# Kernel optimization log

Hardware: AMD Instinct MI355X
Metric: run time of the kernel (lower is better)

## Reference

```python
import jax, jax.numpy as jnp
import numpy as np

E, D, H = 8, 512, 2048  # num_experts, features, features*mlp_ratio
B, S = 4, 512


def _lecun(key, shape):
    fan_in = shape[-2] if len(shape) >= 2 else shape[0]
    return jax.random.normal(key, shape, dtype=jnp.float32) / jnp.sqrt(jnp.float32(fan_in))


def setup_inputs() -> dict:
    key = jax.random.key(0)
    ks = jax.random.split(key, 8)
    return {
        'x_real': jax.random.normal(ks[0], (B, S, D), dtype=jnp.float32),
        'x_imag': jax.random.normal(ks[1], (B, S, D), dtype=jnp.float32),
        # gating Dense over concat([amp, phase]) -> in_features = 2*D
        'gate_W': _lecun(ks[2], (2 * D, E)),
        'gate_b': jnp.zeros((E,), jnp.float32),
        # per-expert ComplexLinear 1: D -> H
        'W1r': _lecun(ks[3], (E, D, H)),
        'W1i': _lecun(ks[4], (E, D, H)),
        'b1r': jnp.zeros((E, H), jnp.float32),
        'b1i': jnp.zeros((E, H), jnp.float32),
        # per-expert ComplexModReLU bias
        'mod_b': jnp.zeros((E, H), jnp.float32),
        # per-expert ComplexLinear 2: H -> D
        'W2r': _lecun(ks[5], (E, H, D)),
        'W2i': _lecun(ks[6], (E, H, D)),
        'b2r': jnp.zeros((E, D), jnp.float32),
        'b2i': jnp.zeros((E, D), jnp.float32),
    }


def reference(x_real, x_imag, gate_W, gate_b, W1r, W1i, b1r, b1i, mod_b, W2r, W2i, b2r, b2i):
    eps = 1e-10
    # --- gating: scores over [|z|, angle(z)] ---
    amp = jnp.sqrt(x_real ** 2 + x_imag ** 2)            # |z|, [B,S,D]
    phase = jnp.arctan2(x_imag, x_real)                  # angle(z)
    routing_input = jnp.concatenate([amp, phase], axis=-1)  # [B,S,2D]
    scores = routing_input @ gate_W + gate_b             # [B,S,E]
    probs = jax.nn.softmax(scores, axis=-1)
    idx = jnp.argmax(probs, axis=-1)                     # [B,S] top-1 expert

    # --- all experts dense (faithful to reference): complex linear 1 ---
    # (Wr + iWi)(xr + ixi) : hr = xr Wr - xi Wi ; hi = xr Wi + xi Wr
    h_r = (jnp.einsum('bsd,edh->ebsh', x_real, W1r)
           - jnp.einsum('bsd,edh->ebsh', x_imag, W1i)) + b1r[:, None, None, :]
    h_i = (jnp.einsum('bsd,edh->ebsh', x_real, W1i)
           + jnp.einsum('bsd,edh->ebsh', x_imag, W1r)) + b1i[:, None, None, :]

    # --- ComplexModReLU: relu(|z|+b) * z / (|z|+eps), |z| = sqrt(r^2+i^2+eps) ---
    a = jnp.sqrt(h_r ** 2 + h_i ** 2 + eps)              # [E,B,S,H]
    scale = jax.nn.relu(a + mod_b[:, None, None, :]) / (a + eps)
    h_r = h_r * scale
    h_i = h_i * scale

    # --- complex linear 2 ---
    o_r = (jnp.einsum('ebsh,ehd->ebsd', h_r, W2r)
           - jnp.einsum('ebsh,ehd->ebsd', h_i, W2i)) + b2r[:, None, None, :]
    o_i = (jnp.einsum('ebsh,ehd->ebsd', h_r, W2i)
           + jnp.einsum('ebsh,ehd->ebsd', h_i, W2r)) + b2i[:, None, None, :]

    # --- mask + weight (top-1): out = sum_e out_e * probs[...,e] * (argmax==e) ---
    e_ids = jnp.arange(probs.shape[-1])
    w = jnp.transpose(probs, (2, 0, 1)) * (idx[None, :, :] == e_ids[:, None, None])  # [E,B,S]
    out_r = jnp.einsum('ebs,ebsd->bsd', w, o_r)
    out_i = jnp.einsum('ebs,ebsd->bsd', w, o_i)
    return (out_r, out_i)
```

## Files before the change

kernel.cpp:

```cpp
#include <hip/hip_runtime.h>
#include <math.h>

#define NE 8
#define ND 512
#define NH 2048
#define NT 2048

typedef __attribute__((ext_vector_type(8))) short short8;
typedef __attribute__((ext_vector_type(4))) float f32x4;

#define GLL(g, d) __builtin_amdgcn_global_load_lds( \
    (const __attribute__((address_space(1))) void*)(g), \
    (__attribute__((address_space(3))) void*)(d), 16, 0, 0)

__device__ __forceinline__ unsigned short f2bf(float x) {
    unsigned int u = __builtin_bit_cast(unsigned int, x);
    u += 0x7FFFu + ((u >> 16) & 1u);
    return (unsigned short)(u >> 16);
}

__device__ __forceinline__ short8 neg8(short8 v) {
    int4 u = __builtin_bit_cast(int4, v);
    u.x ^= 0x80008000; u.y ^= 0x80008000; u.z ^= 0x80008000; u.w ^= 0x80008000;
    return __builtin_bit_cast(short8, u);
}

__device__ __forceinline__ short8 lds8(const unsigned short* p) {
    return *(const short8*)p;
}

__global__ __launch_bounds__(256) void gate_kernel(
    const float* __restrict__ xr, const float* __restrict__ xi,
    const float* __restrict__ gW, const float* __restrict__ gb,
    float* __restrict__ gate_w,
    int* __restrict__ counts, int* __restrict__ tok_list)
{
    int t = blockIdx.x;
    int tid = threadIdx.x;
    const float* xrt = xr + (size_t)t * ND;
    const float* xit = xi + (size_t)t * ND;

    float acc[NE] = {0,0,0,0,0,0,0,0};
    for (int r = tid; r < 2 * ND; r += 256) {
        int d = r & (ND - 1);
        float a = xrt[d], b = xit[d];
        float v = (r < ND) ? sqrtf(a * a + b * b) : atan2f(b, a);
        const float4* g = (const float4*)(gW + (size_t)r * NE);
        float4 g0 = g[0], g1 = g[1];
        acc[0] += v * g0.x; acc[1] += v * g0.y; acc[2] += v * g0.z; acc[3] += v * g0.w;
        acc[4] += v * g1.x; acc[5] += v * g1.y; acc[6] += v * g1.z; acc[7] += v * g1.w;
    }
    #pragma unroll
    for (int e = 0; e < NE; e++) {
        for (int off = 32; off > 0; off >>= 1)
            acc[e] += __shfl_down(acc[e], off, 64);
    }
    __shared__ float part[4][NE];
    int wave = tid >> 6, lane = tid & 63;
    if (lane == 0) {
        #pragma unroll
        for (int e = 0; e < NE; e++) part[wave][e] = acc[e];
    }
    __syncthreads();
    if (tid == 0) {
        float s[NE];
        #pragma unroll
        for (int e = 0; e < NE; e++)
            s[e] = part[0][e] + part[1][e] + part[2][e] + part[3][e] + gb[e];
        int amax = 0; float m = s[0];
        #pragma unroll
        for (int e = 1; e < NE; e++) if (s[e] > m) { m = s[e]; amax = e; }
        float denom = 0.f;
        #pragma unroll
        for (int e = 0; e < NE; e++) denom += expf(s[e] - m);
        gate_w[t] = 1.0f / denom;
        int pos = atomicAdd(&counts[amax], 1);
        tok_list[amax * NT + pos] = t;
    }
}

__global__ __launch_bounds__(256) void convx_kernel(
    const float* __restrict__ xr, const float* __restrict__ xi,
    unsigned short* __restrict__ obr, unsigned short* __restrict__ obi)
{
    int i = blockIdx.x * 256 + threadIdx.x;
    float4 vr = ((const float4*)xr)[i];
    float4 vi = ((const float4*)xi)[i];
    ((ushort4*)obr)[i] = make_ushort4(f2bf(vr.x), f2bf(vr.y), f2bf(vr.z), f2bf(vr.w));
    ((ushort4*)obi)[i] = make_ushort4(f2bf(vi.x), f2bf(vi.y), f2bf(vi.z), f2bf(vi.w));
}

__global__ __launch_bounds__(256) void transw_kernel(
    const float* __restrict__ s0, unsigned short* __restrict__ d0,
    const float* __restrict__ s1, unsigned short* __restrict__ d1,
    int R, int C)
{
    __shared__ float tile[64][65];
    int e = blockIdx.z;
    int c0 = blockIdx.x * 64, r0 = blockIdx.y * 64;
    size_t off = (size_t)e * R * C;
    int tid = threadIdx.x;
    #pragma unroll
    for (int p = 0; p < 2; ++p) {
        const float* src = (p ? s1 : s0) + off;
        unsigned short* dst = (p ? d1 : d0) + off;
        if (p) __syncthreads();
        for (int i = 0; i < 16; ++i) {
            int idx = tid + i * 256;
            int r = idx >> 6, c = idx & 63;
            tile[r][c] = src[(size_t)(r0 + r) * C + c0 + c];
        }
        __syncthreads();
        for (int i = 0; i < 16; ++i) {
            int idx = tid + i * 256;
            int c = idx >> 6, r = idx & 63;
            dst[(size_t)(c0 + c) * R + r0 + r] = f2bf(tile[r][c]);
        }
    }
}

__global__ __launch_bounds__(256, 4) void moe1_kernel(
    const unsigned short* __restrict__ xbr, const unsigned short* __restrict__ xbi,
    const unsigned short* __restrict__ w1tr, const unsigned short* __restrict__ w1ti,
    const float* __restrict__ b1r, const float* __restrict__ b1i,
    const float* __restrict__ mod_b,
    const int* __restrict__ counts, const int* __restrict__ tok_list,
    unsigned short* __restrict__ hr, unsigned short* __restrict__ hi)
{
    int e = blockIdx.z;
    int n = counts[e];
    int mbase = blockIdx.y * 64;
    if (mbase >= n) return;
    int n0 = blockIdx.x * 64;
    int tid = threadIdx.x;
    int w = tid >> 6, l = tid & 63;
    int l15 = l & 15, quad = l >> 4;

    __shared__ unsigned short sAr[64 * 64];
    __shared__ unsigned short sAi[64 * 64];
    __shared__ unsigned short sBr[64 * 64];
    __shared__ unsigned short sBi[64 * 64];
    __shared__ int toks[64];

    const int* tl = tok_list + e * NT;
    if (tid < 64) {
        int idx = mbase + tid;
        toks[tid] = tl[idx < n ? idx : n - 1];
    }
    __syncthreads();

    int swz = (((l & 7) ^ ((l >> 3) & 7)) * 8);
    int ra0 = toks[w * 16 + (l >> 3)];
    int ra1 = toks[w * 16 + 8 + (l >> 3)];
    const unsigned short* gAr0 = xbr + (size_t)ra0 * ND + swz;
    const unsigned short* gAi0 = xbi + (size_t)ra0 * ND + swz;
    const unsigned short* gAr1 = xbr + (size_t)ra1 * ND + swz;
    const unsigned short* gAi1 = xbi + (size_t)ra1 * ND + swz;
    size_t brow = (size_t)e * NH + n0 + w * 16 + (l >> 3);
    const unsigned short* gBr0 = w1tr + brow * ND + swz;
    const unsigned short* gBr1 = w1tr + (brow + 8) * ND + swz;
    const unsigned short* gBi0 = w1ti + brow * ND + swz;
    const unsigned short* gBi1 = w1ti + (brow + 8) * ND + swz;

    unsigned short* dAr0 = sAr + (w * 16) * 64;
    unsigned short* dAr1 = sAr + (w * 16 + 8) * 64;
    unsigned short* dAi0 = sAi + (w * 16) * 64;
    unsigned short* dAi1 = sAi + (w * 16 + 8) * 64;
    unsigned short* dBr0 = sBr + (w * 16) * 64;
    unsigned short* dBr1 = sBr + (w * 16 + 8) * 64;
    unsigned short* dBi0 = sBi + (w * 16) * 64;
    unsigned short* dBi1 = sBi + (w * 16 + 8) * 64;

    f32x4 accr[4] = {}, acci[4] = {};

    for (int kt = 0; kt < ND / 64; ++kt) {
        __syncthreads();
        int ko = kt * 64;
        GLL(gAr0 + ko, dAr0); GLL(gAi0 + ko, dAi0);
        GLL(gAr1 + ko, dAr1); GLL(gAi1 + ko, dAi1);
        GLL(gBr0 + ko, dBr0); GLL(gBr1 + ko, dBr1);
        GLL(gBi0 + ko, dBi0); GLL(gBi1 + ko, dBi1);
        __syncthreads();
        #pragma unroll
        for (int ks = 0; ks < 2; ++ks) {
            int pa = ((ks * 4 + quad) ^ (l15 & 7)) * 8;
            short8 br  = lds8(sBr + (w * 16 + l15) * 64 + pa);
            short8 bi2 = lds8(sBi + (w * 16 + l15) * 64 + pa);
            #pragma unroll
            for (int m = 0; m < 4; ++m) {
                short8 ar  = lds8(sAr + (m * 16 + l15) * 64 + pa);
                short8 ai2 = lds8(sAi + (m * 16 + l15) * 64 + pa);
                short8 an  = neg8(ai2);
                accr[m] = __builtin_amdgcn_mfma_f32_16x16x32_bf16(ar,  br,  accr[m], 0, 0, 0);
                accr[m] = __builtin_amdgcn_mfma_f32_16x16x32_bf16(an,  bi2, accr[m], 0, 0, 0);
                acci[m] = __builtin_amdgcn_mfma_f32_16x16x32_bf16(ar,  bi2, acci[m], 0, 0, 0);
                acci[m] = __builtin_amdgcn_mfma_f32_16x16x32_bf16(ai2, br,  acci[m], 0, 0, 0);
            }
        }
    }

    int col = n0 + w * 16 + l15;
    float bre = b1r[(size_t)e * NH + col];
    float bie = b1i[(size_t)e * NH + col];
    float mbv = mod_b[(size_t)e * NH + col];
    #pragma unroll
    for (int m = 0; m < 4; ++m) {
        #pragma unroll
        for (int r = 0; r < 4; ++r) {
            int tix = m * 16 + quad * 4 + r;
            if (mbase + tix >= n) continue;
            int tok = toks[tix];
            float vr = accr[m][r] + bre;
            float vi = acci[m][r] + bie;
            float a = sqrtf(vr * vr + vi * vi + 1e-10f);
            float sc = fmaxf(a + mbv, 0.0f) / (a + 1e-10f);
            hr[(size_t)tok * NH + col] = f2bf(vr * sc);
            hi[(size_t)tok * NH + col] = f2bf(vi * sc);
        }
    }
}

__global__ __launch_bounds__(256, 4) void moe2_kernel(
    const unsigned short* __restrict__ hr, const unsigned short* __restrict__ hi,
    const unsigned short* __restrict__ w2tr, const unsigned short* __restrict__ w2ti,
    const float* __restrict__ b2r, const float* __restrict__ b2i,
    const int* __restrict__ counts, const int* __restrict__ tok_list,
    const float* __restrict__ gate_w,
    float* __restrict__ out)
{
    int e = blockIdx.z >> 2;
    int ksl = blockIdx.z & 3;
    int n = counts[e];
    int mbase = blockIdx.y * 64;
    if (mbase >= n) return;
    int n0 = blockIdx.x * 64;
    int kbase = ksl * (NH / 4);
    int tid = threadIdx.x;
    int w = tid >> 6, l = tid & 63;
    int l15 = l & 15, quad = l >> 4;

    __shared__ unsigned short sAr[64 * 64];
    __shared__ unsigned short sAi[64 * 64];
    __shared__ unsigned short sBr[64 * 64];
    __shared__ unsigned short sBi[64 * 64];
    __shared__ int toks[64];

    const int* tl = tok_list + e * NT;
    if (tid < 64) {
        int idx = mbase + tid;
        toks[tid] = tl[idx < n ? idx : n - 1];
    }
    __syncthreads();

    int swz = (((l & 7) ^ ((l >> 3) & 7)) * 8);
    int ra0 = toks[w * 16 + (l >> 3)];
    int ra1 = toks[w * 16 + 8 + (l >> 3)];
    const unsigned short* gAr0 = hr + (size_t)ra0 * NH + kbase + swz;
    const unsigned short* gAi0 = hi + (size_t)ra0 * NH + kbase + swz;
    const unsigned short* gAr1 = hr + (size_t)ra1 * NH + kbase + swz;
    const unsigned short* gAi1 = hi + (size_t)ra1 * NH + kbase + swz;
    size_t brow = (size_t)e * ND + n0 + w * 16 + (l >> 3);
    const unsigned short* gBr0 = w2tr + brow * NH + kbase + swz;
    const unsigned short* gBr1 = w2tr + (brow + 8) * NH + kbase + swz;
    const unsigned short* gBi0 = w2ti + brow * NH + kbase + swz;
    const unsigned short* gBi1 = w2ti + (brow + 8) * NH + kbase + swz;

    unsigned short* dAr0 = sAr + (w * 16) * 64;
    unsigned short* dAr1 = sAr + (w * 16 + 8) * 64;
    unsigned short* dAi0 = sAi + (w * 16) * 64;
    unsigned short* dAi1 = sAi + (w * 16 + 8) * 64;
    unsigned short* dBr0 = sBr + (w * 16) * 64;
    unsigned short* dBr1 = sBr + (w * 16 + 8) * 64;
    unsigned short* dBi0 = sBi + (w * 16) * 64;
    unsigned short* dBi1 = sBi + (w * 16 + 8) * 64;

    f32x4 accr[4] = {}, acci[4] = {};

    for (int kt = 0; kt < (NH / 4) / 64; ++kt) {
        __syncthreads();
        int ko = kt * 64;
        GLL(gAr0 + ko, dAr0); GLL(gAi0 + ko, dAi0);
        GLL(gAr1 + ko, dAr1); GLL(gAi1 + ko, dAi1);
        GLL(gBr0 + ko, dBr0); GLL(gBr1 + ko, dBr1);
        GLL(gBi0 + ko, dBi0); GLL(gBi1 + ko, dBi1);
        __syncthreads();
        #pragma unroll
        for (int ks = 0; ks < 2; ++ks) {
            int pa = ((ks * 4 + quad) ^ (l15 & 7)) * 8;
            short8 br  = lds8(sBr + (w * 16 + l15) * 64 + pa);
            short8 bi2 = lds8(sBi + (w * 16 + l15) * 64 + pa);
            #pragma unroll
            for (int m = 0; m < 4; ++m) {
                short8 ar  = lds8(sAr + (m * 16 + l15) * 64 + pa);
                short8 ai2 = lds8(sAi + (m * 16 + l15) * 64 + pa);
                short8 an  = neg8(ai2);
                accr[m] = __builtin_amdgcn_mfma_f32_16x16x32_bf16(ar,  br,  accr[m], 0, 0, 0);
                accr[m] = __builtin_amdgcn_mfma_f32_16x16x32_bf16(an,  bi2, accr[m], 0, 0, 0);
                acci[m] = __builtin_amdgcn_mfma_f32_16x16x32_bf16(ar,  bi2, acci[m], 0, 0, 0);
                acci[m] = __builtin_amdgcn_mfma_f32_16x16x32_bf16(ai2, br,  acci[m], 0, 0, 0);
            }
        }
    }

    int col = n0 + w * 16 + l15;
    float bre = (ksl == 0) ? b2r[(size_t)e * ND + col] : 0.0f;
    float bie = (ksl == 0) ? b2i[(size_t)e * ND + col] : 0.0f;
    #pragma unroll
    for (int m = 0; m < 4; ++m) {
        #pragma unroll
        for (int r = 0; r < 4; ++r) {
            int tix = m * 16 + quad * 4 + r;
            if (mbase + tix >= n) continue;
            int tok = toks[tix];
            float gw = gate_w[tok];
            atomicAdd(&out[(size_t)tok * ND + col], (accr[m][r] + bre) * gw);
            atomicAdd(&out[(size_t)NT * ND + (size_t)tok * ND + col], (acci[m][r] + bie) * gw);
        }
    }
}

extern "C" void kernel_launch(void* const* d_in, const int* in_sizes, int n_in,
                              void* d_out, int out_size, void* d_ws, size_t ws_size,
                              hipStream_t stream) {
    const float* xr   = (const float*)d_in[0];
    const float* xi   = (const float*)d_in[1];
    const float* gW   = (const float*)d_in[2];
    const float* gb   = (const float*)d_in[3];
    const float* W1r  = (const float*)d_in[4];
    const float* W1i  = (const float*)d_in[5];
    const float* b1r  = (const float*)d_in[6];
    const float* b1i  = (const float*)d_in[7];
    const float* modb = (const float*)d_in[8];
    const float* W2r  = (const float*)d_in[9];
    const float* W2i  = (const float*)d_in[10];
    const float* b2r  = (const float*)d_in[11];
    const float* b2i  = (const float*)d_in[12];
    float* out = (float*)d_out;

    char* ws = (char*)d_ws;
    int*   counts   = (int*)ws;
    float* gate_w   = (float*)(ws + 256);
    int*   tok_list = (int*)(ws + 256 + 8192);
    size_t off = 256 + 8192 + (size_t)NE * NT * 4;
    unsigned short* xbr  = (unsigned short*)(ws + off); off += (size_t)NT * ND * 2;
    unsigned short* xbi  = (unsigned short*)(ws + off); off += (size_t)NT * ND * 2;
    unsigned short* w1tr = (unsigned short*)(ws + off); off += (size_t)NE * ND * NH * 2;
    unsigned short* w1ti = (unsigned short*)(ws + off); off += (size_t)NE * ND * NH * 2;
    unsigned short* w2tr = (unsigned short*)(ws + off); off += (size_t)NE * ND * NH * 2;
    unsigned short* w2ti = (unsigned short*)(ws + off); off += (size_t)NE * ND * NH * 2;
    unsigned short* h_r  = (unsigned short*)(ws + off); off += (size_t)NT * NH * 2;
    unsigned short* h_i  = (unsigned short*)(ws + off); off += (size_t)NT * NH * 2;

    hipMemsetAsync(counts, 0, 64 * sizeof(int), stream);
    hipMemsetAsync(out, 0, (size_t)out_size * sizeof(float), stream);
    gate_kernel<<<NT, 256, 0, stream>>>(xr, xi, gW, gb, gate_w, counts, tok_list);
    convx_kernel<<<(NT * ND / 4) / 256, 256, 0, stream>>>(xr, xi, xbr, xbi);
    transw_kernel<<<dim3(NH / 64, ND / 64, NE), 256, 0, stream>>>(W1r, w1tr, W1i, w1ti, ND, NH);
    transw_kernel<<<dim3(ND / 64, NH / 64, NE), 256, 0, stream>>>(W2r, w2tr, W2i, w2ti, NH, ND);
    moe1_kernel<<<dim3(NH / 64, NT / 64, NE), 256, 0, stream>>>(
        xbr, xbi, w1tr, w1ti, b1r, b1i, modb, counts, tok_list, h_r, h_i);
    moe2_kernel<<<dim3(ND / 64, NT / 64, NE * 4), 256, 0, stream>>>(
        h_r, h_i, w2tr, w2ti, b2r, b2i, counts, tok_list, gate_w, out);
}
```

Measured before the change: 314.1 us.

## Switch expert GEMMs to 32x32 MFMA, widen moe1 tile, fuse x conversion, vectorize transpose

Both expert GEMM kernels move from 16x16x32 to 32x32x16 bf16 MFMA with a 2x2 wave layout. moe1 also widens its N tile to 128 columns and drops launch bounds occupancy to 3, aiming for more reuse of each A tile per LDS load. The separate bf16 conversion of x is folded into the gate kernel to save a launch and a reread of x. The weight transpose now converts to bf16 before storing into LDS, uses float4 loads and ushort4 stores, and halves LDS use. The changes add register pressure and lower occupancy, and the fused conversion is done with scalar stores.

```diff
diff --git a/kernel.cpp b/kernel.cpp
--- a/kernel.cpp
+++ b/kernel.cpp
@@ -6,8 +6,8 @@
 #define NH 2048
 #define NT 2048
 
-typedef __attribute__((ext_vector_type(8))) short short8;
-typedef __attribute__((ext_vector_type(4))) float f32x4;
+typedef __attribute__((ext_vector_type(8)))  short short8;
+typedef __attribute__((ext_vector_type(16))) float f32x16;
 
 #define GLL(g, d) __builtin_amdgcn_global_load_lds( \
     (const __attribute__((address_space(1))) void*)(g), \
@@ -33,18 +33,28 @@
     const float* __restrict__ xr, const float* __restrict__ xi,
     const float* __restrict__ gW, const float* __restrict__ gb,
     float* __restrict__ gate_w,
-    int* __restrict__ counts, int* __restrict__ tok_list)
+    int* __restrict__ counts, int* __restrict__ tok_list,
+    unsigned short* __restrict__ xbr, unsigned short* __restrict__ xbi)
 {
     int t = blockIdx.x;
     int tid = threadIdx.x;
     const float* xrt = xr + (size_t)t * ND;
     const float* xit = xi + (size_t)t * ND;
+    unsigned short* obr = xbr + (size_t)t * ND;
+    unsigned short* obi = xbi + (size_t)t * ND;
 
     float acc[NE] = {0,0,0,0,0,0,0,0};
     for (int r = tid; r < 2 * ND; r += 256) {
         int d = r & (ND - 1);
         float a = xrt[d], b = xit[d];
-        float v = (r < ND) ? sqrtf(a * a + b * b) : atan2f(b, a);
+        float v;
+        if (r < ND) {
+            v = sqrtf(a * a + b * b);
+            obr[d] = f2bf(a);
+            obi[d] = f2bf(b);
+        } else {
+            v = atan2f(b, a);
+        }
         const float4* g = (const float4*)(gW + (size_t)r * NE);
         float4 g0 = g[0], g1 = g[1];
         acc[0] += v * g0.x; acc[1] += v * g0.y; acc[2] += v * g0.z; acc[3] += v * g0.w;
@@ -77,17 +87,6 @@
         int pos = atomicAdd(&counts[amax], 1);
         tok_list[amax * NT + pos] = t;
     }
-}
-
-__global__ __launch_bounds__(256) void convx_kernel(
-    const float* __restrict__ xr, const float* __restrict__ xi,
-    unsigned short* __restrict__ obr, unsigned short* __restrict__ obi)
-{
-    int i = blockIdx.x * 256 + threadIdx.x;
-    float4 vr = ((const float4*)xr)[i];
-    float4 vi = ((const float4*)xi)[i];
-    ((ushort4*)obr)[i] = make_ushort4(f2bf(vr.x), f2bf(vr.y), f2bf(vr.z), f2bf(vr.w));
-    ((ushort4*)obi)[i] = make_ushort4(f2bf(vi.x), f2bf(vi.y), f2bf(vi.z), f2bf(vi.w));
 }
 
 __global__ __launch_bounds__(256) void transw_kernel(
@@ -95,31 +94,43 @@
     const float* __restrict__ s1, unsigned short* __restrict__ d1,
     int R, int C)
 {
-    __shared__ float tile[64][65];
+    __shared__ unsigned int tile[64 * 33];
     int e = blockIdx.z;
     int c0 = blockIdx.x * 64, r0 = blockIdx.y * 64;
     size_t off = (size_t)e * R * C;
     int tid = threadIdx.x;
+    int rl = tid >> 4;
+    int c4 = (tid & 15) * 4;
+    int r4 = (tid & 15) * 4;
     #pragma unroll
     for (int p = 0; p < 2; ++p) {
         const float* src = (p ? s1 : s0) + off;
         unsigned short* dst = (p ? d1 : d0) + off;
         if (p) __syncthreads();
-        for (int i = 0; i < 16; ++i) {
-            int idx = tid + i * 256;
-            int r = idx >> 6, c = idx & 63;
-            tile[r][c] = src[(size_t)(r0 + r) * C + c0 + c];
-        }
-        __syncthreads();
-        for (int i = 0; i < 16; ++i) {
-            int idx = tid + i * 256;
-            int c = idx >> 6, r = idx & 63;
-            dst[(size_t)(c0 + c) * R + r0 + r] = f2bf(tile[r][c]);
-        }
-    }
-}
-
-__global__ __launch_bounds__(256, 4) void moe1_kernel(
+        #pragma unroll
+        for (int jj = 0; jj < 4; ++jj) {
+            int r = rl + 16 * jj;
+            float4 v = *(const float4*)(src + (size_t)(r0 + r) * C + c0 + c4);
+            tile[r * 33 + (c4 >> 1)]     = ((unsigned)f2bf(v.y) << 16) | f2bf(v.x);
+            tile[r * 33 + (c4 >> 1) + 1] = ((unsigned)f2bf(v.w) << 16) | f2bf(v.z);
+        }
+        __syncthreads();
+        #pragma unroll
+        for (int ii = 0; ii < 4; ++ii) {
+            int c = (tid >> 4) + 16 * ii;
+            unsigned short o[4];
+            #pragma unroll
+            for (int j = 0; j < 4; ++j) {
+                unsigned int u = tile[(r4 + j) * 33 + (c >> 1)];
+                o[j] = (c & 1) ? (unsigned short)(u >> 16) : (unsigned short)(u & 0xFFFF);
+            }
+            *(ushort4*)(dst + (size_t)(c0 + c) * R + r0 + r4) = make_ushort4(o[0], o[1], o[2], o[3]);
+        }
+        if (p == 0) __syncthreads();
+    }
+}
+
+__global__ __launch_bounds__(256, 3) void moe1_kernel(
     const unsigned short* __restrict__ xbr, const unsigned short* __restrict__ xbi,
     const unsigned short* __restrict__ w1tr, const unsigned short* __restrict__ w1ti,
     const float* __restrict__ b1r, const float* __restrict__ b1i,
@@ -131,15 +142,16 @@
     int n = counts[e];
     int mbase = blockIdx.y * 64;
     if (mbase >= n) return;
-    int n0 = blockIdx.x * 64;
+    int n0 = blockIdx.x * 128;
     int tid = threadIdx.x;
     int w = tid >> 6, l = tid & 63;
-    int l15 = l & 15, quad = l >> 4;
+    int l31 = l & 31, half = l >> 5;
+    int mw = w & 1, nw = w >> 1;
 
     __shared__ unsigned short sAr[64 * 64];
     __shared__ unsigned short sAi[64 * 64];
-    __shared__ unsigned short sBr[64 * 64];
-    __shared__ unsigned short sBi[64 * 64];
+    __shared__ unsigned short sBr[128 * 64];
+    __shared__ unsigned short sBi[128 * 64];
     __shared__ int toks[64];
 
     const int* tl = tok_list + e * NT;
@@ -149,69 +161,84 @@
     }
     __syncthreads();
 
-    int swz = (((l & 7) ^ ((l >> 3) & 7)) * 8);
-    int ra0 = toks[w * 16 + (l >> 3)];
-    int ra1 = toks[w * 16 + 8 + (l >> 3)];
-    const unsigned short* gAr0 = xbr + (size_t)ra0 * ND + swz;
-    const unsigned short* gAi0 = xbi + (size_t)ra0 * ND + swz;
-    const unsigned short* gAr1 = xbr + (size_t)ra1 * ND + swz;
-    const unsigned short* gAi1 = xbi + (size_t)ra1 * ND + swz;
-    size_t brow = (size_t)e * NH + n0 + w * 16 + (l >> 3);
-    const unsigned short* gBr0 = w1tr + brow * ND + swz;
-    const unsigned short* gBr1 = w1tr + (brow + 8) * ND + swz;
-    const unsigned short* gBi0 = w1ti + brow * ND + swz;
-    const unsigned short* gBi1 = w1ti + (brow + 8) * ND + swz;
-
-    unsigned short* dAr0 = sAr + (w * 16) * 64;
-    unsigned short* dAr1 = sAr + (w * 16 + 8) * 64;
-    unsigned short* dAi0 = sAi + (w * 16) * 64;
-    unsigned short* dAi1 = sAi + (w * 16 + 8) * 64;
-    unsigned short* dBr0 = sBr + (w * 16) * 64;
-    unsigned short* dBr1 = sBr + (w * 16 + 8) * 64;
-    unsigned short* dBi0 = sBi + (w * 16) * 64;
-    unsigned short* dBi1 = sBi + (w * 16 + 8) * 64;
-
-    f32x4 accr[4] = {}, acci[4] = {};
+    int c8 = tid & 7;
+    int rloc = tid >> 3;
+    int gc8 = (c8 ^ (rloc & 7)) * 8;
+    int tA0 = toks[rloc], tA1 = toks[rloc + 32];
+    const unsigned short* gAr0 = xbr + (size_t)tA0 * ND + gc8;
+    const unsigned short* gAi0 = xbi + (size_t)tA0 * ND + gc8;
+    const unsigned short* gAr1 = xbr + (size_t)tA1 * ND + gc8;
+    const unsigned short* gAi1 = xbi + (size_t)tA1 * ND + gc8;
+    size_t brow = (size_t)e * NH + n0 + rloc;
+    const unsigned short* gBr0 = w1tr + (brow +  0) * ND + gc8;
+    const unsigned short* gBr1 = w1tr + (brow + 32) * ND + gc8;
+    const unsigned short* gBr2 = w1tr + (brow + 64) * ND + gc8;
+    const unsigned short* gBr3 = w1tr + (brow + 96) * ND + gc8;
+    const unsigned short* gBi0 = w1ti + (brow +  0) * ND + gc8;
+    const unsigned short* gBi1 = w1ti + (brow + 32) * ND + gc8;
+    const unsigned short* gBi2 = w1ti + (brow + 64) * ND + gc8;
+    const unsigned short* gBi3 = w1ti + (brow + 96) * ND + gc8;
+
+    int dA = rloc * 64 + c8 * 8;
+    unsigned short* dAr0 = sAr + dA;          unsigned short* dAr1 = sAr + dA + 32 * 64;
+    unsigned short* dAi0 = sAi + dA;          unsigned short* dAi1 = sAi + dA + 32 * 64;
+    unsigned short* dBr0 = sBr + dA;          unsigned short* dBr1 = sBr + dA + 32 * 64;
+    unsigned short* dBr2 = sBr + dA + 64*64;  unsigned short* dBr3 = sBr + dA + 96 * 64;
+    unsigned short* dBi0 = sBi + dA;          unsigned short* dBi1 = sBi + dA + 32 * 64;
+    unsigned short* dBi2 = sBi + dA + 64*64;  unsigned short* dBi3 = sBi + dA + 96 * 64;
+
+    f32x16 accr[2] = {}, acci[2] = {};
+    int am = mw * 32 + l31;
+    int aoffBase = am * 64;
+    int bn0 = nw * 64 + l31;
+    int bn1 = nw * 64 + 32 + l31;
 
     for (int kt = 0; kt < ND / 64; ++kt) {
         __syncthreads();
         int ko = kt * 64;
-        GLL(gAr0 + ko, dAr0); GLL(gAi0 + ko, dAi0);
-        GLL(gAr1 + ko, dAr1); GLL(gAi1 + ko, dAi1);
+        GLL(gAr0 + ko, dAr0); GLL(gAr1 + ko, dAr1);
+        GLL(gAi0 + ko, dAi0); GLL(gAi1 + ko, dAi1);
         GLL(gBr0 + ko, dBr0); GLL(gBr1 + ko, dBr1);
+        GLL(gBr2 + ko, dBr2); GLL(gBr3 + ko, dBr3);
         GLL(gBi0 + ko, dBi0); GLL(gBi1 + ko, dBi1);
-        __syncthreads();
-        #pragma unroll
-        for (int ks = 0; ks < 2; ++ks) {
-            int pa = ((ks * 4 + quad) ^ (l15 & 7)) * 8;
-            short8 br  = lds8(sBr + (w * 16 + l15) * 64 + pa);
-            short8 bi2 = lds8(sBi + (w * 16 + l15) * 64 + pa);
-            #pragma unroll
-            for (int m = 0; m < 4; ++m) {
-                short8 ar  = lds8(sAr + (m * 16 + l15) * 64 + pa);
-                short8 ai2 = lds8(sAi + (m * 16 + l15) * 64 + pa);
-                short8 an  = neg8(ai2);
-                accr[m] = __builtin_amdgcn_mfma_f32_16x16x32_bf16(ar,  br,  accr[m], 0, 0, 0);
-                accr[m] = __builtin_amdgcn_mfma_f32_16x16x32_bf16(an,  bi2, accr[m], 0, 0, 0);
-                acci[m] = __builtin_amdgcn_mfma_f32_16x16x32_bf16(ar,  bi2, acci[m], 0, 0, 0);
-                acci[m] = __builtin_amdgcn_mfma_f32_16x16x32_bf16(ai2, br,  acci[m], 0, 0, 0);
-            }
-        }
-    }
-
-    int col = n0 + w * 16 + l15;
-    float bre = b1r[(size_t)e * NH + col];
-    float bie = b1i[(size_t)e * NH + col];
-    float mbv = mod_b[(size_t)e * NH + col];
+        GLL(gBi2 + ko, dBi2); GLL(gBi3 + ko, dBi3);
+        __syncthreads();
+        #pragma unroll
+        for (int ks = 0; ks < 4; ++ks) {
+            int kc = ks * 2 + half;
+            int ao = aoffBase + ((kc ^ (am & 7)) * 8);
+            short8 ar = lds8(sAr + ao);
+            short8 ai = lds8(sAi + ao);
+            short8 an = neg8(ai);
+            int bo0 = bn0 * 64 + ((kc ^ (bn0 & 7)) * 8);
+            int bo1 = bn1 * 64 + ((kc ^ (bn1 & 7)) * 8);
+            short8 br0 = lds8(sBr + bo0), bi0 = lds8(sBi + bo0);
+            short8 br1 = lds8(sBr + bo1), bi1 = lds8(sBi + bo1);
+            accr[0] = __builtin_amdgcn_mfma_f32_32x32x16_bf16(ar, br0, accr[0], 0, 0, 0);
+            accr[0] = __builtin_amdgcn_mfma_f32_32x32x16_bf16(an, bi0, accr[0], 0, 0, 0);
+            acci[0] = __builtin_amdgcn_mfma_f32_32x32x16_bf16(ar, bi0, acci[0], 0, 0, 0);
+            acci[0] = __builtin_amdgcn_mfma_f32_32x32x16_bf16(ai, br0, acci[0], 0, 0, 0);
+            accr[1] = __builtin_amdgcn_mfma_f32_32x32x16_bf16(ar, br1, accr[1], 0, 0, 0);
+            accr[1] = __builtin_amdgcn_mfma_f32_32x32x16_bf16(an, bi1, accr[1], 0, 0, 0);
+            acci[1] = __builtin_amdgcn_mfma_f32_32x32x16_bf16(ar, bi1, acci[1], 0, 0, 0);
+            acci[1] = __builtin_amdgcn_mfma_f32_32x32x16_bf16(ai, br1, acci[1], 0, 0, 0);
+        }
+    }
+
     #pragma unroll
-    for (int m = 0; m < 4; ++m) {
-        #pragma unroll
-        for (int r = 0; r < 4; ++r) {
-            int tix = m * 16 + quad * 4 + r;
+    for (int ns = 0; ns < 2; ++ns) {
+        int col = n0 + nw * 64 + ns * 32 + l31;
+        float bre = b1r[(size_t)e * NH + col];
+        float bie = b1i[(size_t)e * NH + col];
+        float mbv = mod_b[(size_t)e * NH + col];
+        #pragma unroll
+        for (int reg = 0; reg < 16; ++reg) {
+            int row = (reg & 3) + 8 * (reg >> 2) + 4 * half;
+            int tix = mw * 32 + row;
             if (mbase + tix >= n) continue;
             int tok = toks[tix];
-            float vr = accr[m][r] + bre;
-            float vi = acci[m][r] + bie;
+            float vr = accr[ns][reg] + bre;
+            float vi = acci[ns][reg] + bie;
             float a = sqrtf(vr * vr + vi * vi + 1e-10f);
             float sc = fmaxf(a + mbv, 0.0f) / (a + 1e-10f);
             hr[(size_t)tok * NH + col] = f2bf(vr * sc);
@@ -237,7 +264,8 @@
     int kbase = ksl * (NH / 4);
     int tid = threadIdx.x;
     int w = tid >> 6, l = tid & 63;
-    int l15 = l & 15, quad = l >> 4;
+    int l31 = l & 31, half = l >> 5;
+    int mw = w & 1, nw = w >> 1;
 
     __shared__ unsigned short sAr[64 * 64];
     __shared__ unsigned short sAi[64 * 64];
@@ -252,70 +280,68 @@
     }
     __syncthreads();
 
-    int swz = (((l & 7) ^ ((l >> 3) & 7)) * 8);
-    int ra0 = toks[w * 16 + (l >> 3)];
-    int ra1 = toks[w * 16 + 8 + (l >> 3)];
-    const unsigned short* gAr0 = hr + (size_t)ra0 * NH + kbase + swz;
-    const unsigned short* gAi0 = hi + (size_t)ra0 * NH + kbase + swz;
-    const unsigned short* gAr1 = hr + (size_t)ra1 * NH + kbase + swz;
-    const unsigned short* gAi1 = hi + (size_t)ra1 * NH + kbase + swz;
-    size_t brow = (size_t)e * ND + n0 + w * 16 + (l >> 3);
-    const unsigned short* gBr0 = w2tr + brow * NH + kbase + swz;
-    const unsigned short* gBr1 = w2tr + (brow + 8) * NH + kbase + swz;
-    const unsigned short* gBi0 = w2ti + brow * NH + kbase + swz;
-    const unsigned short* gBi1 = w2ti + (brow + 8) * NH + kbase + swz;
-
-    unsigned short* dAr0 = sAr + (w * 16) * 64;
-    unsigned short* dAr1 = sAr + (w * 16 + 8) * 64;
-    unsigned short* dAi0 = sAi + (w * 16) * 64;
-    unsigned short* dAi1 = sAi + (w * 16 + 8) * 64;
-    unsigned short* dBr0 = sBr + (w * 16) * 64;
-    unsigned short* dBr1 = sBr + (w * 16 + 8) * 64;
-    unsigned short* dBi0 = sBi + (w * 16) * 64;
-    unsigned short* dBi1 = sBi + (w * 16 + 8) * 64;
-
-    f32x4 accr[4] = {}, acci[4] = {};
+    int c8 = tid & 7;
+    int rloc = tid >> 3;
+    int gc8 = (c8 ^ (rloc & 7)) * 8;
+    int tA0 = toks[rloc], tA1 = toks[rloc + 32];
+    const unsigned short* gAr0 = hr + (size_t)tA0 * NH + kbase + gc8;
+    const unsigned short* gAi0 = hi + (size_t)tA0 * NH + kbase + gc8;
+    const unsigned short* gAr1 = hr + (size_t)tA1 * NH + kbase + gc8;
+    const unsigned short* gAi1 = hi + (size_t)tA1 * NH + kbase + gc8;
+    size_t brow = (size_t)e * ND + n0 + rloc;
+    const unsigned short* gBr0 = w2tr + (brow +  0) * NH + kbase + gc8;
+    const unsigned short* gBr1 = w2tr + (brow + 32) * NH + kbase + gc8;
+    const unsigned short* gBi0 = w2ti + (brow +  0) * NH + kbase + gc8;
+    const unsigned short* gBi1 = w2ti + (brow + 32) * NH + kbase + gc8;
+
+    int dA = rloc * 64 + c8 * 8;
+    unsigned short* dAr0 = sAr + dA; unsigned short* dAr1 = sAr + dA + 32 * 64;
+    unsigned short* dAi0 = sAi + dA; unsigned short* dAi1 = sAi + dA + 32 * 64;
+    unsigned short* dBr0 = sBr + dA; unsigned short* dBr1 = sBr + dA + 32 * 64;
+    unsigned short* dBi0 = sBi + dA; unsigned short* dBi1 = sBi + dA + 32 * 64;
+
+    f32x16 accr = {}, acci = {};
+    int am = mw * 32 + l31;
+    int aoffBase = am * 64;
+    int bn = nw * 32 + l31;
+    int boffBase = bn * 64;
 
     for (int kt = 0; kt < (NH / 4) / 64; ++kt) {
         __syncthreads();
         int ko = kt * 64;
-        GLL(gAr0 + ko, dAr0); GLL(gAi0 + ko, dAi0);
-        GLL(gAr1 + ko, dAr1); GLL(gAi1 + ko, dAi1);
+        GLL(gAr0 + ko, dAr0); GLL(gAr1 + ko, dAr1);
+        GLL(gAi0 + ko, dAi0); GLL(gAi1 + ko, dAi1);
         GLL(gBr0 + ko, dBr0); GLL(gBr1 + ko, dBr1);
         GLL(gBi0 + ko, dBi0); GLL(gBi1 + ko, dBi1);
         __syncthreads();
         #pragma unroll
-        for (int ks = 0; ks < 2; ++ks) {
-            int pa = ((ks * 4 + quad) ^ (l15 & 7)) * 8;
-            short8 br  = lds8(sBr + (w * 16 + l15) * 64 + pa);
-            short8 bi2 = lds8(sBi + (w * 16 + l15) * 64 + pa);
-            #pragma unroll
-            for (int m = 0; m < 4; ++m) {
-                short8 ar  = lds8(sAr + (m * 16 + l15) * 64 + pa);
-                short8 ai2 = lds8(sAi + (m * 16 + l15) * 64 + pa);
-                short8 an  = neg8(ai2);
-                accr[m] = __builtin_amdgcn_mfma_f32_16x16x32_bf16(ar,  br,  accr[m], 0, 0, 0);
-                accr[m] = __builtin_amdgcn_mfma_f32_16x16x32_bf16(an,  bi2, accr[m], 0, 0, 0);
-                acci[m] = __builtin_amdgcn_mfma_f32_16x16x32_bf16(ar,  bi2, acci[m], 0, 0, 0);
-                acci[m] = __builtin_amdgcn_mfma_f32_16x16x32_bf16(ai2, br,  acci[m], 0, 0, 0);
-            }
-        }
-    }
-
-    int col = n0 + w * 16 + l15;
+        for (int ks = 0; ks < 4; ++ks) {
+            int kc = ks * 2 + half;
+            int ao = aoffBase + ((kc ^ (am & 7)) * 8);
+            short8 ar = lds8(sAr + ao);
+            short8 ai = lds8(sAi + ao);
+            short8 an = neg8(ai);
+            int bo = boffBase + ((kc ^ (bn & 7)) * 8);
+            short8 br = lds8(sBr + bo), bi = lds8(sBi + bo);
+            accr = __builtin_amdgcn_mfma_f32_32x32x16_bf16(ar, br, accr, 0, 0, 0);
+            accr = __builtin_amdgcn_mfma_f32_32x32x16_bf16(an, bi, accr, 0, 0, 0);
+            acci = __builtin_amdgcn_mfma_f32_32x32x16_bf16(ar, bi, acci, 0, 0, 0);
+            acci = __builtin_amdgcn_mfma_f32_32x32x16_bf16(ai, br, acci, 0, 0, 0);
+        }
+    }
+
+    int col = n0 + nw * 32 + l31;
     float bre = (ksl == 0) ? b2r[(size_t)e * ND + col] : 0.0f;
     float bie = (ksl == 0) ? b2i[(size_t)e * ND + col] : 0.0f;
     #pragma unroll
-    for (int m = 0; m < 4; ++m) {
-        #pragma unroll
-        for (int r = 0; r < 4; ++r) {
-            int tix = m * 16 + quad * 4 + r;
-            if (mbase + tix >= n) continue;
-            int tok = toks[tix];
-            float gw = gate_w[tok];
-            atomicAdd(&out[(size_t)tok * ND + col], (accr[m][r] + bre) * gw);
-            atomicAdd(&out[(size_t)NT * ND + (size_t)tok * ND + col], (acci[m][r] + bie) * gw);
-        }
+    for (int reg = 0; reg < 16; ++reg) {
+        int row = (reg & 3) + 8 * (reg >> 2) + 4 * half;
+        int tix = mw * 32 + row;
+        if (mbase + tix >= n) continue;
+        int tok = toks[tix];
+        float gw = gate_w[tok];
+        atomicAdd(&out[(size_t)tok * ND + col], (accr[reg] + bre) * gw);
+        atomicAdd(&out[(size_t)NT * ND + (size_t)tok * ND + col], (acci[reg] + bie) * gw);
     }
 }
 
@@ -353,11 +379,10 @@
 
     hipMemsetAsync(counts, 0, 64 * sizeof(int), stream);
     hipMemsetAsync(out, 0, (size_t)out_size * sizeof(float), stream);
-    gate_kernel<<<NT, 256, 0, stream>>>(xr, xi, gW, gb, gate_w, counts, tok_list);
-    convx_kernel<<<(NT * ND / 4) / 256, 256, 0, stream>>>(xr, xi, xbr, xbi);
+    gate_kernel<<<NT, 256, 0, stream>>>(xr, xi, gW, gb, gate_w, counts, tok_list, xbr, xbi);
     transw_kernel<<<dim3(NH / 64, ND / 64, NE), 256, 0, stream>>>(W1r, w1tr, W1i, w1ti, ND, NH);
     transw_kernel<<<dim3(ND / 64, NH / 64, NE), 256, 0, stream>>>(W2r, w2tr, W2i, w2ti, NH, ND);
-    moe1_kernel<<<dim3(NH / 64, NT / 64, NE), 256, 0, stream>>>(
+    moe1_kernel<<<dim3(NH / 128, NT / 64, NE), 256, 0, stream>>>(
         xbr, xbi, w1tr, w1ti, b1r, b1i, modb, counts, tok_list, h_r, h_i);
     moe2_kernel<<<dim3(ND / 64, NT / 64, NE * 4), 256, 0, stream>>>(
         h_r, h_i, w2tr, w2ti, b2r, b2i, counts, tok_list, gate_w, out);
```

New measurement: 318.2 us. About the same (+1.3%).
